# Kernel tuning notes

Hardware: AMD Instinct MI355X
Metric: run time of the kernel (lower is better)

Reference implementation:

```python
import jax, jax.numpy as jnp
import numpy as np

B, T, C, H = 4, 2048, 1024, 1024

def setup_inputs() -> dict:
    key = jax.random.key(0)
    ks = jax.random.split(key, 7)
    s = 0.02
    return {
        "x": jax.random.normal(ks[0], (B, T, C), dtype=jnp.float32),
        "k": jax.random.normal(ks[1], (B, T, C), dtype=jnp.float32),
        "q": jax.random.normal(ks[2], (B, T, C), dtype=jnp.float32),
        "v": jax.random.normal(ks[3], (B, T, C), dtype=jnp.float32),
        "Wk": jax.random.normal(ks[4], (C, H), dtype=jnp.float32) * s,
        "Wq": jax.random.normal(ks[5], (C, H), dtype=jnp.float32) * s,
        "Wv": jax.random.normal(ks[6], (C, H), dtype=jnp.float32) * s,
    }

def reference(x, k, q, v, Wk, Wq, Wv):
    Tcur = x.shape[1]
    kp = jnp.einsum('btc,ch->bth', k, Wk)
    qp = jnp.einsum('btc,ch->bth', q, Wq)
    # NOTE: original torch code (faithfully) projects v with the QUERY weights
    vp = jnp.einsum('btc,ch->bth', v, Wq)
    scale = jnp.asarray(H, jnp.float32) ** -0.5
    weights = jnp.einsum('bth,bsh->bts', qp, kp) * scale  # [B,T,T]
    causal = jnp.tril(jnp.ones((Tcur, Tcur), dtype=bool))
    weights = jnp.where(causal, weights, -jnp.inf)
    weights = jax.nn.softmax(weights, axis=-1)
    # dropout p=0.0 -> identity
    out = jnp.einsum('bts,bsh->bth', weights, vp)
    return out
```

## Files before the change

kernel.cpp:

```cpp
#include <hip/hip_runtime.h>
#include <stdint.h>
#include <math.h>

typedef unsigned short u16;
typedef __attribute__((ext_vector_type(8))) short short8;
typedef __attribute__((ext_vector_type(8))) u16 ushort8;
typedef __attribute__((ext_vector_type(4))) u16 u16x4;
typedef __attribute__((ext_vector_type(4))) float floatx4;

__device__ __forceinline__ u16 f2bf(float f) {
  union { float f; unsigned u; } c; c.f = f;
  unsigned u = c.u;
  return (u16)((u + 0x7fffu + ((u >> 16) & 1u)) >> 16);
}
__device__ __forceinline__ float bf2f(u16 h) {
  union { unsigned u; float f; } c; c.u = (unsigned)h << 16;
  return c.f;
}

__device__ __forceinline__ void async16(const u16* g, u16* l) {
  auto* gp = reinterpret_cast<const __attribute__((address_space(1))) uint32_t*>(
      reinterpret_cast<uintptr_t>(g));
  auto* lp = reinterpret_cast<__attribute__((address_space(3))) uint32_t*>(
      reinterpret_cast<uintptr_t>(l));
  __builtin_amdgcn_global_load_lds(gp, lp, 16, 0, 0);
}

#define WAIT_VM4 0xF74
#define WAIT_VM0 0xF70

template <int OUT_BF16, int SPLITK>
__global__ __launch_bounds__(256) void gemm_bt(
    const u16* __restrict__ A, const u16* __restrict__ B, void* __restrict__ Cv,
    int K, int lda, int ldb, int ldc,
    long long sA, long long sB, long long sC,
    float scale, int tri_grid, int causal_klimit,
    int vpt, u16* __restrict__ vpC) {
  int bm, bn;
  int kt0 = 0;
  bool part0_heavy = false;
  bool atomic_out = false;
  if (tri_grid) {
    const int bx = blockIdx.x;
    int i = (int)((sqrtf(8.f * bx + 1.f) - 1.f) * 0.5f);
    while ((i + 1) * (i + 2) / 2 <= bx) ++i;
    while (i * (i + 1) / 2 > bx) --i;
    bm = i;
    bn = bx - i * (i + 1) / 2;
  } else if (SPLITK) {
    const int bx = blockIdx.x;
    if (bx < 8) {
      bm = 8 + bx; part0_heavy = true; atomic_out = true;
    } else if (bx < 16) {
      bm = 15 - (bx - 8); kt0 = 32; atomic_out = true;
    } else {
      bm = 23 - bx;
    }
    bn = blockIdx.y;
  } else {
    bm = blockIdx.x;
    bn = blockIdx.y;
  }
  const int m0 = bm * 128;
  const int n0 = bn * 128;
  A += (size_t)blockIdx.z * sA;
  B += (size_t)blockIdx.z * sB;

  __shared__ u16 As[2][4096];
  __shared__ u16 Bs[2][4096];

  const int tid = threadIdx.x;
  const int lane = tid & 63;
  const int wid = tid >> 6;
  const int wm = (wid & 1) * 64;
  const int wn = (wid >> 1) * 64;
  const int fr = lane & 15;
  const int fq = lane >> 4;

  floatx4 acc[4][4] = {};

  int kt_end = K >> 5;
  if (causal_klimit) {
    int lim = (m0 >> 5) + 4;
    if (lim < kt_end) kt_end = lim;
  }
  if (part0_heavy && kt_end > 32) kt_end = 32;

  const int rowi = tid >> 2;
  const int segi = tid & 3;
  const int sgz = segi ^ ((rowi >> 1) & 3);
  const u16* gA = A + (size_t)(m0 + rowi) * lda + sgz * 8;
  const u16* gB = B + (size_t)(n0 + rowi) * ldb + sgz * 8;

  int offA[4], offB[4];
#pragma unroll
  for (int i = 0; i < 4; ++i) {
    int ra = wm + i * 16 + fr;
    offA[i] = ra * 32 + (fq ^ ((ra >> 1) & 3)) * 8;
    int rb = wn + i * 16 + fr;
    offB[i] = rb * 32 + (fq ^ ((rb >> 1) & 3)) * 8;
  }

  auto issue = [&](int kt) {
    const int k0 = kt << 5;
    const int odd = kt & 1;
    async16(gA + k0, &As[odd][tid * 8]);
    async16(gA + k0 + (size_t)64 * lda, &As[odd][tid * 8 + 2048]);
    async16(gB + k0, &Bs[odd][tid * 8]);
    async16(gB + k0 + (size_t)64 * ldb, &Bs[odd][tid * 8 + 2048]);
  };

  issue(kt0);
  for (int kt = kt0; kt < kt_end; ++kt) {
    if (kt + 1 < kt_end) {
      issue(kt + 1);
      __builtin_amdgcn_s_waitcnt(WAIT_VM4);
    } else {
      __builtin_amdgcn_s_waitcnt(WAIT_VM0);
    }
    asm volatile("s_barrier" ::: "memory");

    const u16* ab = As[kt & 1];
    const u16* bb = Bs[kt & 1];
    short8 av[4], bv[4];
#pragma unroll
    for (int i = 0; i < 4; ++i) av[i] = *(const short8*)(ab + offA[i]);
#pragma unroll
    for (int j = 0; j < 4; ++j) bv[j] = *(const short8*)(bb + offB[j]);

#pragma unroll
    for (int i = 0; i < 4; ++i)
#pragma unroll
      for (int j = 0; j < 4; ++j)
        acc[i][j] = __builtin_amdgcn_mfma_f32_16x16x32_bf16(av[i], bv[j],
                                                            acc[i][j], 0, 0, 0);
    asm volatile("s_barrier" ::: "memory");
  }

  if (vpt && blockIdx.z == 2) {
#pragma unroll
    for (int i = 0; i < 4; ++i) {
      const int m = m0 + wm + i * 16 + fq * 4;
      const int b = m >> 11, t = m & 2047;
#pragma unroll
      for (int j = 0; j < 4; ++j) {
        const int n = n0 + wn + j * 16 + fr;
        u16x4 o;
#pragma unroll
        for (int r = 0; r < 4; ++r) o[r] = f2bf(acc[i][j][r]);
        *(u16x4*)&vpC[(size_t)b * 2097152 + (size_t)n * 2048 + t] = o;
      }
    }
    return;
  }
  if (OUT_BF16) {
    u16* C = (u16*)Cv + (size_t)blockIdx.z * sC;
#pragma unroll
    for (int i = 0; i < 4; ++i) {
      const int m = m0 + wm + i * 16 + fq * 4;
#pragma unroll
      for (int j = 0; j < 4; ++j) {
        const int n = n0 + wn + j * 16 + fr;
#pragma unroll
        for (int r = 0; r < 4; ++r)
          C[(size_t)(m + r) * ldc + n] = f2bf(acc[i][j][r] * scale);
      }
    }
  } else {
    float* C = (float*)Cv + (size_t)blockIdx.z * sC;
    if (SPLITK && atomic_out) {
#pragma unroll
      for (int i = 0; i < 4; ++i) {
        const int m = m0 + wm + i * 16 + fq * 4;
#pragma unroll
        for (int j = 0; j < 4; ++j) {
          const int n = n0 + wn + j * 16 + fr;
#pragma unroll
          for (int r = 0; r < 4; ++r)
            unsafeAtomicAdd(&C[(size_t)(m + r) * ldc + n],
                            acc[i][j][r] * scale);
        }
      }
    } else {
#pragma unroll
      for (int i = 0; i < 4; ++i) {
        const int m = m0 + wm + i * 16 + fq * 4;
#pragma unroll
        for (int j = 0; j < 4; ++j) {
          const int n = n0 + wn + j * 16 + fr;
#pragma unroll
          for (int r = 0; r < 4; ++r)
            C[(size_t)(m + r) * ldc + n] = acc[i][j][r] * scale;
        }
      }
    }
  }
}

__global__ __launch_bounds__(256) void prep(
    const float* __restrict__ q, const float* __restrict__ k,
    const float* __restrict__ v, const float* __restrict__ Wq,
    const float* __restrict__ Wk, u16* __restrict__ qkv,
    u16* __restrict__ WT, float* __restrict__ out) {
  __shared__ u16 tile[64][72];
  const int bx = blockIdx.x;
  const int tid = threadIdx.x;

  if (bx < 12288) {
    const int z = bx >> 12;
    const int i = (bx & 4095) * 256 + tid;
    const float* src = z == 0 ? q : (z == 1 ? k : v);
    u16* dst = qkv + (size_t)z * 8388608;
    floatx4 a = ((const floatx4*)src)[i * 2];
    floatx4 b = ((const floatx4*)src)[i * 2 + 1];
    ushort8 o;
#pragma unroll
    for (int j = 0; j < 4; ++j) { o[j] = f2bf(a[j]); o[4 + j] = f2bf(b[j]); }
    ((ushort8*)dst)[i] = o;
    return;
  }
  if (bx < 13056) {
    const int idx = bx - 12288;
    const int zw = idx >> 8;
    const int rem = idx & 255;
    const int r0 = (rem >> 4) * 64;
    const int c0 = (rem & 15) * 64;
    const int R = 1024, C = 1024;
    const float* in = (zw == 1) ? Wk : Wq;
    u16* dst = WT + (size_t)zw * R * C;
#pragma unroll
    for (int rnd = 0; rnd < 2; ++rnd) {
      int e = rnd * 256 + tid;
      int rr = e >> 3, seg = e & 7;
      const float* p = &in[(size_t)(r0 + rr) * C + c0 + seg * 8];
      floatx4 a = *(const floatx4*)p;
      floatx4 b = *(const floatx4*)(p + 4);
      u16* tp = &tile[rr][seg * 8];
#pragma unroll
      for (int j = 0; j < 4; ++j) { tp[j] = f2bf(a[j]); tp[4 + j] = f2bf(b[j]); }
    }
    __syncthreads();
#pragma unroll
    for (int rnd = 0; rnd < 2; ++rnd) {
      int e = rnd * 256 + tid;
      int cc = e >> 3, rseg = e & 7;
      ushort8 tv;
#pragma unroll
      for (int j = 0; j < 8; ++j) tv[j] = tile[rseg * 8 + j][cc];
      *(ushort8*)&dst[(size_t)(c0 + cc) * R + r0 + rseg * 8] = tv;
    }
    return;
  }
  {
    const size_t i = (size_t)(bx - 13056) * 256 + tid;
    const size_t z = i >> 18;
    const size_t r = i & 262143;
    floatx4* p = (floatx4*)(out + z * 2097152 + 1048576) + r;
    *p = floatx4{0.f, 0.f, 0.f, 0.f};
  }
}

__global__ __launch_bounds__(256) void softmax_causal(u16* __restrict__ S,
                                                      int T) {
  const int row = blockIdx.x * 4 + (threadIdx.x >> 6);
  const int t = row & (T - 1);
  const int len = t + 1;
  u16* srow = S + (size_t)row * T;
  const int lane = threadIdx.x & 63;

  ushort8 raw0 = *(const ushort8*)(srow + (lane) * 8);
  ushort8 raw1 = *(const ushort8*)(srow + (64 + lane) * 8);
  ushort8 raw2 = *(const ushort8*)(srow + (128 + lane) * 8);
  ushort8 raw3 = *(const ushort8*)(srow + (192 + lane) * 8);

  float v0[8], v1[8], v2[8], v3[8];
  float mx = -1e30f;
#pragma unroll
  for (int j = 0; j < 8; ++j) {
    const int i0 = lane * 8 + j;
    v0[j] = (i0 < len) ? bf2f(raw0[j]) : -1e30f;
    v1[j] = (i0 + 512 < len) ? bf2f(raw1[j]) : -1e30f;
    v2[j] = (i0 + 1024 < len) ? bf2f(raw2[j]) : -1e30f;
    v3[j] = (i0 + 1536 < len) ? bf2f(raw3[j]) : -1e30f;
    mx = fmaxf(mx, fmaxf(fmaxf(v0[j], v1[j]), fmaxf(v2[j], v3[j])));
  }
#pragma unroll
  for (int o = 32; o > 0; o >>= 1) mx = fmaxf(mx, __shfl_xor(mx, o, 64));

  float sum = 0.f;
#pragma unroll
  for (int j = 0; j < 8; ++j) {
    v0[j] = __expf(v0[j] - mx); sum += v0[j];
    v1[j] = __expf(v1[j] - mx); sum += v1[j];
    v2[j] = __expf(v2[j] - mx); sum += v2[j];
    v3[j] = __expf(v3[j] - mx); sum += v3[j];
  }
#pragma unroll
  for (int o = 32; o > 0; o >>= 1) sum += __shfl_xor(sum, o, 64);
  const float inv = 1.f / sum;

  ushort8 o0, o1, o2, o3;
#pragma unroll
  for (int j = 0; j < 8; ++j) {
    o0[j] = f2bf(v0[j] * inv);
    o1[j] = f2bf(v1[j] * inv);
    o2[j] = f2bf(v2[j] * inv);
    o3[j] = f2bf(v3[j] * inv);
  }
  *(ushort8*)(srow + (lane) * 8) = o0;
  *(ushort8*)(srow + (64 + lane) * 8) = o1;
  *(ushort8*)(srow + (128 + lane) * 8) = o2;
  *(ushort8*)(srow + (192 + lane) * 8) = o3;
}

extern "C" void kernel_launch(void* const* d_in, const int* in_sizes, int n_in,
                              void* d_out, int out_size, void* d_ws,
                              size_t ws_size, hipStream_t stream) {
  (void)in_sizes; (void)n_in; (void)out_size; (void)ws_size;
  const float* k  = (const float*)d_in[1];
  const float* q  = (const float*)d_in[2];
  const float* v  = (const float*)d_in[3];
  const float* Wk = (const float*)d_in[4];
  const float* Wq = (const float*)d_in[5];
  float* out = (float*)d_out;

  const int B = 4, T = 2048, C = 1024, H = 1024;
  const int M = B * T;
  const size_t MC = (size_t)M * C, CH = (size_t)C * H, MH = (size_t)M * H;

  u16* qkv  = (u16*)d_ws;
  u16* WT   = qkv + 3 * MC;
  u16* qkvp = WT + 3 * CH;
  u16* vpT  = qkvp + 2 * MH;
  u16* Sb   = vpT + MH;

  prep<<<dim3(17152), 256, 0, stream>>>(q, k, v, Wq, Wk, qkv, WT, out);

  gemm_bt<1, 0><<<dim3(M / 128, H / 128, 3), 256, 0, stream>>>(
      qkv, WT, qkvp, C, C, C, H,
      (long long)MC, (long long)CH, (long long)MH, 1.f, 0, 0, 1, vpT);

  gemm_bt<1, 0><<<dim3(136, 1, B), 256, 0, stream>>>(
      qkvp, qkvp + MH, Sb, H, H, H, T,
      (long long)T * H, (long long)T * H, (long long)T * T,
      0.03125f, 1, 0, 0, nullptr);

  softmax_causal<<<dim3(B * T / 4), 256, 0, stream>>>(Sb, T);

  gemm_bt<0, 1><<<dim3(24, H / 128, B), 256, 0, stream>>>(
      Sb, vpT, out, T, T, T, H,
      (long long)T * T, (long long)H * T, (long long)T * H,
      1.f, 0, 1, 0, nullptr);
}
```

Baseline: 324.7 us.

## Fold Wk into Wq via precomputed Wq·Wkᵀ, skip key projection GEMM

Precomputes a combined C×C matrix from Wq and Wk with a small GEMM, so the query projection directly yields q·Wq·Wkᵀ and scores are computed against raw bf16 keys. This removes the separate key projection GEMM (one third of the projection work) at the cost of an extra 1024³ GEMM and an added bf16 rounding of the fused weight. It also remaps the triangular score grid's block order to interleave heavy and light tiles across dispatch order for load balance.

```diff
diff --git a/kernel.cpp b/kernel.cpp
--- a/kernel.cpp
+++ b/kernel.cpp
@@ -41,7 +41,8 @@
   bool part0_heavy = false;
   bool atomic_out = false;
   if (tri_grid) {
-    const int bx = blockIdx.x;
+    int bx = blockIdx.x;
+    bx = (bx & 7) * 17 + (bx >> 3);
     int i = (int)((sqrtf(8.f * bx + 1.f) - 1.f) * 0.5f);
     while ((i + 1) * (i + 2) / 2 <= bx) ++i;
     while (i * (i + 1) / 2 > bx) --i;
@@ -137,7 +138,7 @@
     asm volatile("s_barrier" ::: "memory");
   }
 
-  if (vpt && blockIdx.z == 2) {
+  if (vpt && (int)blockIdx.z == vpt) {
 #pragma unroll
     for (int i = 0; i < 4; ++i) {
       const int m = m0 + wm + i * 16 + fq * 4;
@@ -219,15 +220,27 @@
     ((ushort8*)dst)[i] = o;
     return;
   }
-  if (bx < 13056) {
+  if (bx < 13312) {
     const int idx = bx - 12288;
-    const int zw = idx >> 8;
-    const int rem = idx & 255;
+    const int w = idx >> 9;
+    const int i = (idx & 511) * 256 + tid;
+    const float* src = w ? Wk : Wq;
+    u16* dst = WT + (size_t)(2 + w) * 1048576;
+    floatx4 a = ((const floatx4*)src)[i * 2];
+    floatx4 b = ((const floatx4*)src)[i * 2 + 1];
+    ushort8 o;
+#pragma unroll
+    for (int j = 0; j < 4; ++j) { o[j] = f2bf(a[j]); o[4 + j] = f2bf(b[j]); }
+    ((ushort8*)dst)[i] = o;
+    return;
+  }
+  if (bx < 13568) {
+    const int rem = bx - 13312;
     const int r0 = (rem >> 4) * 64;
     const int c0 = (rem & 15) * 64;
     const int R = 1024, C = 1024;
-    const float* in = (zw == 1) ? Wk : Wq;
-    u16* dst = WT + (size_t)zw * R * C;
+    const float* in = Wq;
+    u16* dst = WT + 1048576;
 #pragma unroll
     for (int rnd = 0; rnd < 2; ++rnd) {
       int e = rnd * 256 + tid;
@@ -252,7 +265,7 @@
     return;
   }
   {
-    const size_t i = (size_t)(bx - 13056) * 256 + tid;
+    const size_t i = (size_t)(bx - 13568) * 256 + tid;
     const size_t z = i >> 18;
     const size_t r = i & 262143;
     floatx4* p = (floatx4*)(out + z * 2097152 + 1048576) + r;
@@ -330,19 +343,23 @@
 
   u16* qkv  = (u16*)d_ws;
   u16* WT   = qkv + 3 * MC;
-  u16* qkvp = WT + 3 * CH;
-  u16* vpT  = qkvp + 2 * MH;
+  u16* qkvp = WT + 4 * CH;
+  u16* vpT  = qkvp + MH;
   u16* Sb   = vpT + MH;
 
-  prep<<<dim3(17152), 256, 0, stream>>>(q, k, v, Wq, Wk, qkv, WT, out);
-
-  gemm_bt<1, 0><<<dim3(M / 128, H / 128, 3), 256, 0, stream>>>(
+  prep<<<dim3(17664), 256, 0, stream>>>(q, k, v, Wq, Wk, qkv, WT, out);
+
+  gemm_bt<1, 0><<<dim3(8, 8, 1), 256, 0, stream>>>(
+      WT + 3 * CH, WT + 2 * CH, WT, C, C, C, C,
+      0, 0, 0, 1.f, 0, 0, 0, nullptr);
+
+  gemm_bt<1, 0><<<dim3(M / 128, H / 128, 2), 256, 0, stream>>>(
       qkv, WT, qkvp, C, C, C, H,
-      (long long)MC, (long long)CH, (long long)MH, 1.f, 0, 0, 1, vpT);
+      (long long)(2 * MC), (long long)CH, 0, 1.f, 0, 0, 1, vpT);
 
   gemm_bt<1, 0><<<dim3(136, 1, B), 256, 0, stream>>>(
-      qkvp, qkvp + MH, Sb, H, H, H, T,
-      (long long)T * H, (long long)T * H, (long long)T * T,
+      qkvp, qkv + MC, Sb, C, H, C, T,
+      (long long)T * H, (long long)T * C, (long long)T * T,
       0.03125f, 1, 0, 0, nullptr);
 
   softmax_causal<<<dim3(B * T / 4), 256, 0, stream>>>(Sb, T);
```

Measured after the change: 307.5 us. -5.3%, faster.

## Fold Wk into query-side weight and convert fp32 operands inside GEMM loaders

Applied to the files above, without the earlier changes.

The code reassociates q·Wq·(k·Wk)^T as q·(Wq·Wk^T)·k^T. A small 1024^3 GEMM builds the combined weight, and the separate k projection disappears. The fp32 inputs q, v and k are now read directly in the GEMM loaders and converted to bf16 into LDS, which removes the large standalone conversion pass and its bf16 workspace round trip. The triangular grid is also remapped to interleave heavy and light tiles. The cost is register-staged, non-async fp32 loads with double the global bytes per tile, plus an extra rounding step on the combined weight that changes numerics slightly.

```diff
diff --git a/kernel.cpp b/kernel.cpp
--- a/kernel.cpp
+++ b/kernel.cpp
@@ -26,22 +26,26 @@
   __builtin_amdgcn_global_load_lds(gp, lp, 16, 0, 0);
 }
 
+#define WAIT_VM6 0xF76
 #define WAIT_VM4 0xF74
 #define WAIT_VM0 0xF70
 
-template <int OUT_BF16, int SPLITK>
+template <int OUT_BF16, int SPLITK, int A32, int B32>
 __global__ __launch_bounds__(256) void gemm_bt(
     const u16* __restrict__ A, const u16* __restrict__ B, void* __restrict__ Cv,
     int K, int lda, int ldb, int ldc,
     long long sA, long long sB, long long sC,
     float scale, int tri_grid, int causal_klimit,
-    int vpt, u16* __restrict__ vpC) {
+    int vpt, u16* __restrict__ vpC,
+    const float* __restrict__ Afp, const float* __restrict__ Afp2,
+    const float* __restrict__ Bfp) {
   int bm, bn;
   int kt0 = 0;
   bool part0_heavy = false;
   bool atomic_out = false;
   if (tri_grid) {
-    const int bx = blockIdx.x;
+    int bx = blockIdx.x;
+    bx = (bx & 7) * 17 + (bx >> 3);
     int i = (int)((sqrtf(8.f * bx + 1.f) - 1.f) * 0.5f);
     while ((i + 1) * (i + 2) / 2 <= bx) ++i;
     while (i * (i + 1) / 2 > bx) --i;
@@ -63,8 +67,8 @@
   }
   const int m0 = bm * 128;
   const int n0 = bn * 128;
-  A += (size_t)blockIdx.z * sA;
-  B += (size_t)blockIdx.z * sB;
+  if (!A32) A += (size_t)blockIdx.z * sA;
+  if (!B32) B += (size_t)blockIdx.z * sB;
 
   __shared__ u16 As[2][4096];
   __shared__ u16 Bs[2][4096];
@@ -89,8 +93,23 @@
   const int rowi = tid >> 2;
   const int segi = tid & 3;
   const int sgz = segi ^ ((rowi >> 1) & 3);
-  const u16* gA = A + (size_t)(m0 + rowi) * lda + sgz * 8;
-  const u16* gB = B + (size_t)(n0 + rowi) * ldb + sgz * 8;
+  const u16* gA = nullptr;
+  const u16* gB = nullptr;
+  const float* gAf = nullptr;
+  const float* gBf = nullptr;
+  if (A32) {
+    const float* Af = (Afp2 && blockIdx.z == 1)
+                          ? Afp2
+                          : (Afp + (size_t)blockIdx.z * sA);
+    gAf = Af + (size_t)(m0 + rowi) * lda + sgz * 8;
+  } else {
+    gA = A + (size_t)(m0 + rowi) * lda + sgz * 8;
+  }
+  if (B32) {
+    gBf = Bfp + (size_t)blockIdx.z * sB + (size_t)(n0 + rowi) * ldb + sgz * 8;
+  } else {
+    gB = B + (size_t)(n0 + rowi) * ldb + sgz * 8;
+  }
 
   int offA[4], offB[4];
 #pragma unroll
@@ -101,23 +120,74 @@
     offB[i] = rb * 32 + (fq ^ ((rb >> 1) & 3)) * 8;
   }
 
-  auto issue = [&](int kt) {
+  auto issueA = [&](int kt) {
     const int k0 = kt << 5;
     const int odd = kt & 1;
     async16(gA + k0, &As[odd][tid * 8]);
     async16(gA + k0 + (size_t)64 * lda, &As[odd][tid * 8 + 2048]);
+  };
+  auto issueB = [&](int kt) {
+    const int k0 = kt << 5;
+    const int odd = kt & 1;
     async16(gB + k0, &Bs[odd][tid * 8]);
     async16(gB + k0 + (size_t)64 * ldb, &Bs[odd][tid * 8 + 2048]);
   };
 
-  issue(kt0);
+  floatx4 rA[4], rB[4];
+  auto loadA32 = [&](int kt) {
+    const float* s = gAf + (kt << 5);
+    rA[0] = *(const floatx4*)s;
+    rA[1] = *(const floatx4*)(s + 4);
+    rA[2] = *(const floatx4*)(s + (size_t)64 * lda);
+    rA[3] = *(const floatx4*)(s + (size_t)64 * lda + 4);
+  };
+  auto storeA32 = [&](int kt) {
+    const int odd = kt & 1;
+    ushort8 o0, o1;
+#pragma unroll
+    for (int m = 0; m < 4; ++m) {
+      o0[m] = f2bf(rA[0][m]); o0[4 + m] = f2bf(rA[1][m]);
+      o1[m] = f2bf(rA[2][m]); o1[4 + m] = f2bf(rA[3][m]);
+    }
+    *(ushort8*)&As[odd][tid * 8] = o0;
+    *(ushort8*)&As[odd][tid * 8 + 2048] = o1;
+  };
+  auto loadB32 = [&](int kt) {
+    const float* s = gBf + (kt << 5);
+    rB[0] = *(const floatx4*)s;
+    rB[1] = *(const floatx4*)(s + 4);
+    rB[2] = *(const floatx4*)(s + (size_t)64 * ldb);
+    rB[3] = *(const floatx4*)(s + (size_t)64 * ldb + 4);
+  };
+  auto storeB32 = [&](int kt) {
+    const int odd = kt & 1;
+    ushort8 o0, o1;
+#pragma unroll
+    for (int m = 0; m < 4; ++m) {
+      o0[m] = f2bf(rB[0][m]); o0[4 + m] = f2bf(rB[1][m]);
+      o1[m] = f2bf(rB[2][m]); o1[4 + m] = f2bf(rB[3][m]);
+    }
+    *(ushort8*)&Bs[odd][tid * 8] = o0;
+    *(ushort8*)&Bs[odd][tid * 8 + 2048] = o1;
+  };
+
+  if (A32) loadA32(kt0); else issueA(kt0);
+  if (B32) loadB32(kt0); else issueB(kt0);
   for (int kt = kt0; kt < kt_end; ++kt) {
+    if (A32) storeA32(kt);
+    if (B32) storeB32(kt);
     if (kt + 1 < kt_end) {
-      issue(kt + 1);
-      __builtin_amdgcn_s_waitcnt(WAIT_VM4);
+      if (A32) loadA32(kt + 1); else issueA(kt + 1);
+      if (B32) loadB32(kt + 1); else issueB(kt + 1);
+      if (!A32 && !B32) {
+        __builtin_amdgcn_s_waitcnt(WAIT_VM4);
+      } else if (!(A32 && B32)) {
+        __builtin_amdgcn_s_waitcnt(WAIT_VM6);
+      }
     } else {
-      __builtin_amdgcn_s_waitcnt(WAIT_VM0);
-    }
+      if (!(A32 && B32)) __builtin_amdgcn_s_waitcnt(WAIT_VM0);
+    }
+    if (A32 || B32) asm volatile("s_waitcnt lgkmcnt(0)" ::: "memory");
     asm volatile("s_barrier" ::: "memory");
 
     const u16* ab = As[kt & 1];
@@ -137,7 +207,7 @@
     asm volatile("s_barrier" ::: "memory");
   }
 
-  if (vpt && blockIdx.z == 2) {
+  if (vpt && (int)blockIdx.z == vpt) {
 #pragma unroll
     for (int i = 0; i < 4; ++i) {
       const int m = m0 + wm + i * 16 + fq * 4;
@@ -198,46 +268,28 @@
 }
 
 __global__ __launch_bounds__(256) void prep(
-    const float* __restrict__ q, const float* __restrict__ k,
-    const float* __restrict__ v, const float* __restrict__ Wq,
-    const float* __restrict__ Wk, u16* __restrict__ qkv,
-    u16* __restrict__ WT, float* __restrict__ out) {
+    const float* __restrict__ Wq, u16* __restrict__ WT,
+    float* __restrict__ out) {
   __shared__ u16 tile[64][72];
   const int bx = blockIdx.x;
   const int tid = threadIdx.x;
 
-  if (bx < 12288) {
-    const int z = bx >> 12;
-    const int i = (bx & 4095) * 256 + tid;
-    const float* src = z == 0 ? q : (z == 1 ? k : v);
-    u16* dst = qkv + (size_t)z * 8388608;
-    floatx4 a = ((const floatx4*)src)[i * 2];
-    floatx4 b = ((const floatx4*)src)[i * 2 + 1];
-    ushort8 o;
-#pragma unroll
-    for (int j = 0; j < 4; ++j) { o[j] = f2bf(a[j]); o[4 + j] = f2bf(b[j]); }
-    ((ushort8*)dst)[i] = o;
-    return;
-  }
-  if (bx < 13056) {
-    const int idx = bx - 12288;
-    const int zw = idx >> 8;
-    const int rem = idx & 255;
-    const int r0 = (rem >> 4) * 64;
-    const int c0 = (rem & 15) * 64;
+  if (bx < 256) {
+    const int r0 = (bx >> 4) * 64;
+    const int c0 = (bx & 15) * 64;
     const int R = 1024, C = 1024;
-    const float* in = (zw == 1) ? Wk : Wq;
-    u16* dst = WT + (size_t)zw * R * C;
+    u16* dstT = WT + 1048576;
 #pragma unroll
     for (int rnd = 0; rnd < 2; ++rnd) {
       int e = rnd * 256 + tid;
       int rr = e >> 3, seg = e & 7;
-      const float* p = &in[(size_t)(r0 + rr) * C + c0 + seg * 8];
+      const float* p = &Wq[(size_t)(r0 + rr) * C + c0 + seg * 8];
       floatx4 a = *(const floatx4*)p;
       floatx4 b = *(const floatx4*)(p + 4);
-      u16* tp = &tile[rr][seg * 8];
-#pragma unroll
-      for (int j = 0; j < 4; ++j) { tp[j] = f2bf(a[j]); tp[4 + j] = f2bf(b[j]); }
+      ushort8 o;
+#pragma unroll
+      for (int j = 0; j < 4; ++j) { o[j] = f2bf(a[j]); o[4 + j] = f2bf(b[j]); }
+      *(ushort8*)&tile[rr][seg * 8] = o;
     }
     __syncthreads();
 #pragma unroll
@@ -247,16 +299,20 @@
       ushort8 tv;
 #pragma unroll
       for (int j = 0; j < 8; ++j) tv[j] = tile[rseg * 8 + j][cc];
-      *(ushort8*)&dst[(size_t)(c0 + cc) * R + r0 + rseg * 8] = tv;
+      *(ushort8*)&dstT[(size_t)(c0 + cc) * R + r0 + rseg * 8] = tv;
     }
     return;
   }
   {
-    const size_t i = (size_t)(bx - 13056) * 256 + tid;
-    const size_t z = i >> 18;
-    const size_t r = i & 262143;
-    floatx4* p = (floatx4*)(out + z * 2097152 + 1048576) + r;
-    *p = floatx4{0.f, 0.f, 0.f, 0.f};
+    const int blk = bx - 256;
+#pragma unroll
+    for (int j = 0; j < 4; ++j) {
+      const size_t i = (size_t)blk * 1024 + j * 256 + tid;
+      const size_t z = i >> 18;
+      const size_t r = i & 262143;
+      *((floatx4*)(out + z * 2097152 + 1048576) + r) =
+          floatx4{0.f, 0.f, 0.f, 0.f};
+    }
   }
 }
 
@@ -326,29 +382,32 @@
 
   const int B = 4, T = 2048, C = 1024, H = 1024;
   const int M = B * T;
-  const size_t MC = (size_t)M * C, CH = (size_t)C * H, MH = (size_t)M * H;
-
-  u16* qkv  = (u16*)d_ws;
-  u16* WT   = qkv + 3 * MC;
-  u16* qkvp = WT + 3 * CH;
-  u16* vpT  = qkvp + 2 * MH;
+  const size_t CH = (size_t)C * H, MH = (size_t)M * H;
+
+  u16* WT   = (u16*)d_ws;
+  u16* qkvp = WT + 2 * CH;
+  u16* vpT  = qkvp + MH;
   u16* Sb   = vpT + MH;
 
-  prep<<<dim3(17152), 256, 0, stream>>>(q, k, v, Wq, Wk, qkv, WT, out);
-
-  gemm_bt<1, 0><<<dim3(M / 128, H / 128, 3), 256, 0, stream>>>(
-      qkv, WT, qkvp, C, C, C, H,
-      (long long)MC, (long long)CH, (long long)MH, 1.f, 0, 0, 1, vpT);
-
-  gemm_bt<1, 0><<<dim3(136, 1, B), 256, 0, stream>>>(
-      qkvp, qkvp + MH, Sb, H, H, H, T,
-      (long long)T * H, (long long)T * H, (long long)T * T,
-      0.03125f, 1, 0, 0, nullptr);
+  prep<<<dim3(1280), 256, 0, stream>>>(Wq, WT, out);
+
+  gemm_bt<1, 0, 1, 1><<<dim3(8, 8, 1), 256, 0, stream>>>(
+      nullptr, nullptr, WT, C, C, C, C, 0, 0, 0,
+      1.f, 0, 0, 0, nullptr, Wk, nullptr, Wq);
+
+  gemm_bt<1, 0, 1, 0><<<dim3(M / 128, H / 128, 2), 256, 0, stream>>>(
+      nullptr, WT, qkvp, C, C, C, H, 0, (long long)CH, 0,
+      1.f, 0, 0, 1, vpT, q, v, nullptr);
+
+  gemm_bt<1, 0, 0, 1><<<dim3(136, 1, B), 256, 0, stream>>>(
+      qkvp, nullptr, Sb, C, H, C, T,
+      (long long)T * H, (long long)T * C, (long long)T * T,
+      0.03125f, 1, 0, 0, nullptr, nullptr, nullptr, k);
 
   softmax_causal<<<dim3(B * T / 4), 256, 0, stream>>>(Sb, T);
 
-  gemm_bt<0, 1><<<dim3(24, H / 128, B), 256, 0, stream>>>(
+  gemm_bt<0, 1, 0, 0><<<dim3(24, H / 128, B), 256, 0, stream>>>(
       Sb, vpT, out, T, T, T, H,
       (long long)T * T, (long long)H * T, (long long)T * H,
-      1.f, 0, 1, 0, nullptr);
-}
+      1.f, 0, 1, 0, nullptr, nullptr, nullptr, nullptr);
+}
```

New measurement: 344.2 us. +6.0%, slower.
